# Performance work log

Hardware: AMD Instinct MI355X
Metric: run time of the kernel (lower is better)

The kernel has to match this reference:

```python
import jax, jax.numpy as jnp
import numpy as np


def _consts():
    # Hypercube vertices: itertools.product([-1,1], repeat=n) order => MSB-first bits.
    def verts(nbits):
        idx = np.arange(2 ** nbits)
        return (((idx[:, None] >> np.arange(nbits - 1, -1, -1)[None, :]) & 1) * 2.0 - 1.0).astype(np.float32)

    hexagrams = verts(6)   # (64, 6)
    q2_verts = verts(2)    # (4, 2)
    q3_verts = verts(3)    # (8, 3)

    # Q2 vertex -> group one-hot, _Q2_TO_GROUP = [2, 1, 1, 0]
    q2_to_group = np.zeros((4, 3), dtype=np.float32)
    for v, g in enumerate([2, 1, 1, 0]):
        q2_to_group[v, g] = 1.0

    # Group anchors: ABSTRACT = mean(hex[63], hex[62]), DYNAMIC = mean(hex[19], hex[21]),
    # CONCRETE = mean(hex[0], hex[8]); then L2-normalized.
    anch = np.stack([
        hexagrams[[63, 62]].mean(0),
        hexagrams[[19, 21]].mean(0),
        hexagrams[[0, 8]].mean(0),
    ]).astype(np.float32)
    anch = anch / np.clip(np.linalg.norm(anch, axis=-1, keepdims=True), 1e-12, None)

    # Walsh-Hadamard popcount masks, pre-divided by their sums -> (64, 3) matrix.
    bits = np.array([bin(i).count('1') for i in range(64)], dtype=np.float32)
    wa = (bits >= 5).astype(np.float32)
    wd = (bits == 3).astype(np.float32)
    wc = (bits <= 1).astype(np.float32)
    wht_mat = np.stack([wa / wa.sum(), wd / wd.sum(), wc / wc.sum()], axis=1)

    return tuple(jnp.asarray(a) for a in (hexagrams, q2_verts, q3_verts, q2_to_group, anch, wht_mat))


def _q3_to_group_init():
    q3_map = np.zeros((8, 3), dtype=np.float32)
    for i in range(8):
        yc = bin(i).count('1')
        if yc == 0:
            q3_map[i, 2] = 1.0
        elif yc == 1:
            q3_map[i, 1] = 1.0
        elif yc == 2:
            q3_map[i, 0] = 0.6
            q3_map[i, 1] = 0.4
        else:
            q3_map[i, 0] = 1.0
    q3_map = q3_map / np.clip(q3_map.sum(axis=1, keepdims=True), 1e-8, None)
    return q3_map


def setup_inputs() -> dict:
    key = jax.random.key(0)
    k_x, k2, k3, k6 = jax.random.split(key, 4)
    B, T, D = 4, 4096, 2048
    s = 1.0 / float(np.sqrt(D))  # torch Linear default init range
    return {
        'x': jax.random.normal(k_x, (B, T, D), dtype=jnp.float32),
        'ln_w': jnp.ones((D,), dtype=jnp.float32),
        'ln_b': jnp.zeros((D,), dtype=jnp.float32),
        'w_q2': jax.random.uniform(k2, (2, D), minval=-s, maxval=s, dtype=jnp.float32),
        'w_q3': jax.random.uniform(k3, (3, D), minval=-s, maxval=s, dtype=jnp.float32),
        'w_q6': jax.random.uniform(k6, (6, D), minval=-s, maxval=s, dtype=jnp.float32),
        'log_temp': jnp.asarray(np.log(0.5), dtype=jnp.float32),
        'log_scale_mix': jnp.zeros((3,), dtype=jnp.float32),
        'q3_to_group': jnp.asarray(_q3_to_group_init()),
        'log_wht_mix': jnp.asarray(-2.0, dtype=jnp.float32),
    }


def _forward(x, ln_w, ln_b, w_q2, w_q3, w_q6, log_temp, log_scale_mix, q3_to_group, log_wht_mix):
    hexa, q2v, q3v, q2g, anch, wht_mat = _consts()

    # LayerNorm (eps = 1e-5, torch default)
    mu = x.mean(-1, keepdims=True)
    var = ((x - mu) ** 2).mean(-1, keepdims=True)
    h = (x - mu) * jax.lax.rsqrt(var + 1e-5) * ln_w + ln_b

    temp = jnp.clip(jnp.exp(log_temp), 0.1, 5.0)

    # Q2 scale: (B,T,2) -> 4 vertices -> 3 groups
    w2 = jax.nn.softmax(jnp.tanh(h @ w_q2.T) @ q2v.T / temp, axis=-1)
    score_q2 = w2 @ q2g

    # Q3 scale: (B,T,3) -> 8 vertices -> learned soft group map
    w3 = jax.nn.softmax(jnp.tanh(h @ w_q3.T) @ q3v.T / temp, axis=-1)
    score_q3 = w3 @ jax.nn.softmax(q3_to_group, axis=-1)

    # Q6 scale: (B,T,6) -> 64 hexagram vertices
    hex_w = jax.nn.softmax(jnp.tanh(h @ w_q6.T) @ hexa.T / temp, axis=-1)
    score_cos = (hex_w @ hexa) @ anch.T            # cosine-sim vs normalized anchors
    score_wht = hex_w @ wht_mat                    # popcount-mask averages
    alpha = jax.nn.sigmoid(log_wht_mix)
    score_q6 = (1.0 - alpha) * score_cos + alpha * score_wht

    mix = jax.nn.softmax(log_scale_mix)
    group_w = jax.nn.softmax(mix[0] * score_q2 + mix[1] * score_q3 + mix[2] * score_q6, axis=-1)

    mg = group_w.mean(axis=(0, 1))
    mh = hex_w.mean(axis=(0, 1))
    lb_loss = jnp.sum(mg * jnp.log(mg + 1e-8)) + 0.1 * jnp.sum(mh * jnp.log(mh + 1e-8))
    return group_w, hex_w, lb_loss


def reference(x, ln_w, ln_b, w_q2, w_q3, w_q6, log_temp, log_scale_mix, q3_to_group, log_wht_mix):
    return _forward(x, ln_w, ln_b, w_q2, w_q3, w_q6, log_temp, log_scale_mix, q3_to_group, log_wht_mix)
```

## Files before the change

### kernel.cpp

```cpp
#include <hip/hip_runtime.h>
#include <math.h>
#include <string.h>

#define D 2048
#define NTOK 16384
#define NROW 11
#define MROWS_U32 (NROW * D / 2)
#define K1_BLOCKS 1024
#define K1_THREADS 256
#define WROWS 13
#define WSTRIDE_U 1032
#define TILE_S 20

#define WS_A 0
#define WS_B 16
#define WS_IT 32
#define WS_ALPHA 33
#define WS_MIX 34
#define WS_M3 40
#define WS_MERGED 64
#define WS_PART (WS_MERGED + MROWS_U32)

typedef __fp16 h2 __attribute__((ext_vector_type(2)));
typedef __fp16 h8 __attribute__((ext_vector_type(8)));
typedef float f32x4 __attribute__((ext_vector_type(4)));

__device__ __forceinline__ float wsum(float v){
#pragma unroll
  for (int m = 1; m < 64; m <<= 1) v += __shfl_xor(v, m, 64);
  return v;
}
__device__ __forceinline__ float wmax(float v){
#pragma unroll
  for (int m = 1; m < 64; m <<= 1) v = fmaxf(v, __shfl_xor(v, m, 64));
  return v;
}
__device__ __forceinline__ float rcp_fast(float x){ return __builtin_amdgcn_rcpf(x); }
__device__ __forceinline__ float tanh_fast(float x){
  float e = __expf(2.0f * x);
  return 1.0f - 2.0f * rcp_fast(e + 1.0f);
}
__device__ __forceinline__ float sload(const float* __restrict__ p){
  return __uint_as_float(__builtin_amdgcn_readfirstlane(__float_as_uint(*p)));
}
__device__ __forceinline__ unsigned int h2u(h2 h){ unsigned int u; memcpy(&u, &h, 4); return u; }

__global__ __launch_bounds__(256) void k0_prep(
    const float* __restrict__ ln_w, const float* __restrict__ ln_b,
    const float* __restrict__ w_q2, const float* __restrict__ w_q3,
    const float* __restrict__ w_q6,
    const float* __restrict__ log_temp, const float* __restrict__ log_scale_mix,
    const float* __restrict__ q3_to_group, const float* __restrict__ log_wht_mix,
    float* __restrict__ ws)
{
  const int tid = threadIdx.x;
  const int k = blockIdx.x;
  unsigned int* wsu = (unsigned int*)ws;
  if (k < NROW){
    const float* row = (k < 2) ? (w_q2 + (size_t)k * D)
                     : (k < 5) ? (w_q3 + (size_t)(k - 2) * D)
                               : (w_q6 + (size_t)(k - 5) * D);
    float pa = 0.f, pb = 0.f;
    for (int i = tid * 2; i < D; i += 512){
      float w0 = row[i], w1 = row[i + 1];
      h2 h = __builtin_amdgcn_cvt_pkrtz(ln_w[i] * w0, ln_w[i + 1] * w1);
      pa += (float)h[0] + (float)h[1];
      pb = fmaf(ln_b[i], w0, pb);
      pb = fmaf(ln_b[i + 1], w1, pb);
      wsu[WS_MERGED + k * 1024 + i / 2] = h2u(h);
    }
    __shared__ float red[8];
    pa = wsum(pa); pb = wsum(pb);
    if ((tid & 63) == 0){ red[tid >> 6] = pa; red[4 + (tid >> 6)] = pb; }
    __syncthreads();
    if (tid == 0){
      ws[WS_A + k] = red[0] + red[1] + red[2] + red[3];
      ws[WS_B + k] = red[4] + red[5] + red[6] + red[7];
    }
  } else if (tid == 0){
    float t = __expf(log_temp[0]);
    t = fminf(fmaxf(t, 0.1f), 5.0f);
    ws[WS_IT] = 1.0f / t;
    ws[WS_ALPHA] = 1.0f / (1.0f + __expf(-log_wht_mix[0]));
    float m0 = log_scale_mix[0], m1 = log_scale_mix[1], m2 = log_scale_mix[2];
    float mm = fmaxf(m0, fmaxf(m1, m2));
    float e0 = __expf(m0 - mm), e1 = __expf(m1 - mm), e2 = __expf(m2 - mm);
    float inv = 1.0f / (e0 + e1 + e2);
    ws[WS_MIX + 0] = e0 * inv; ws[WS_MIX + 1] = e1 * inv; ws[WS_MIX + 2] = e2 * inv;
    for (int r = 0; r < 8; ++r){
      float v0 = q3_to_group[r*3+0], v1 = q3_to_group[r*3+1], v2 = q3_to_group[r*3+2];
      float mx = fmaxf(v0, fmaxf(v1, v2));
      float f0 = __expf(v0 - mx), f1 = __expf(v1 - mx), f2 = __expf(v2 - mx);
      float iv = 1.0f / (f0 + f1 + f2);
      ws[WS_M3 + r*3 + 0] = f0 * iv;
      ws[WS_M3 + r*3 + 1] = f1 * iv;
      ws[WS_M3 + r*3 + 2] = f2 * iv;
    }
  }
}

__global__ __launch_bounds__(256) void k1_main(
    const float* __restrict__ x, const float* __restrict__ ws,
    float* __restrict__ gout, float* __restrict__ hout, float* __restrict__ part)
{
  __shared__ unsigned int sW[WROWS * WSTRIDE_U];
  __shared__ float tile[4][16][TILE_S];
  __shared__ float lred[4][68];
  const int tid  = threadIdx.x;
  const int lane = tid & 63;
  const int wid  = tid >> 6;
  const int blk  = blockIdx.x;
  const int tok0 = blk * 16;
  const int n = lane & 15;
  const int q = lane >> 4;

  {
    const uint4* src = (const uint4*)((const unsigned int*)ws + WS_MERGED);
    const uint4 ones4 = make_uint4(0x3C003C00u, 0x3C003C00u, 0x3C003C00u, 0x3C003C00u);
    const uint4 zero4 = make_uint4(0u, 0u, 0u, 0u);
#pragma unroll
    for (int j = 0; j < WROWS; ++j){
      int idx = tid + j * 256;
      int r = idx >> 8, i = idx & 255;
      uint4 v = (r < NROW) ? src[r * 256 + i] : ((r == NROW) ? ones4 : zero4);
      *(uint4*)(sW + r * WSTRIDE_U + i * 4) = v;
    }
  }

  const float* xp = x + (size_t)(tok0 + n) * D + wid * 512 + q * 8;

  f32x4 acc = {0.f, 0.f, 0.f, 0.f};
  float sq = 0.f;

  float4 f0 = *(const float4*)(xp);
  float4 f1 = *(const float4*)(xp + 4);

  __syncthreads();

  const int wr = (n <= 12) ? n : 12;
  const unsigned int* wb = sW + wr * WSTRIDE_U + wid * 256 + q * 4;

#pragma unroll
  for (int s = 0; s < 16; ++s){
    float4 g0, g1;
    if (s < 15){
      g0 = *(const float4*)(xp + (s + 1) * 32);
      g1 = *(const float4*)(xp + (s + 1) * 32 + 4);
    }
    sq = fmaf(f0.x,f0.x, fmaf(f0.y,f0.y, fmaf(f0.z,f0.z, fmaf(f0.w,f0.w, sq))));
    sq = fmaf(f1.x,f1.x, fmaf(f1.y,f1.y, fmaf(f1.z,f1.z, fmaf(f1.w,f1.w, sq))));
    h2 p0 = __builtin_amdgcn_cvt_pkrtz(f0.x, f0.y);
    h2 p1 = __builtin_amdgcn_cvt_pkrtz(f0.z, f0.w);
    h2 p2 = __builtin_amdgcn_cvt_pkrtz(f1.x, f1.y);
    h2 p3 = __builtin_amdgcn_cvt_pkrtz(f1.z, f1.w);
    h8 A;
    A[0]=p0[0]; A[1]=p0[1]; A[2]=p1[0]; A[3]=p1[1];
    A[4]=p2[0]; A[5]=p2[1]; A[6]=p3[0]; A[7]=p3[1];
    uint4 wq = *(const uint4*)(wb + s * 16);
    h8 B; memcpy(&B, &wq, 16);
    acc = __builtin_amdgcn_mfma_f32_16x16x32_f16(A, B, acc, 0, 0, 0);
    f0 = g0; f1 = g1;
  }

  sq += __shfl_xor(sq, 16, 64);
  sq += __shfl_xor(sq, 32, 64);

#pragma unroll
  for (int r = 0; r < 4; ++r) tile[wid][q * 4 + r][n] = acc[r];
  if (lane < 16) tile[wid][lane][16] = sq;

  __syncthreads();

  float a[NROW], bb[NROW];
#pragma unroll
  for (int k = 0; k < NROW; ++k){ a[k] = sload(ws + WS_A + k); bb[k] = sload(ws + WS_B + k); }
  const float it    = sload(ws + WS_IT);
  const float alpha = sload(ws + WS_ALPHA);
  const float mix0 = sload(ws + WS_MIX), mix1 = sload(ws + WS_MIX + 1), mix2 = sload(ws + WS_MIX + 2);
  float M3r[8][3];
#pragma unroll
  for (int r = 0; r < 8; ++r){
#pragma unroll
    for (int g = 0; g < 3; ++g) M3r[r][g] = sload(ws + WS_M3 + r*3 + g);
  }

  float sgn[6];
#pragma unroll
  for (int j = 0; j < 6; ++j) sgn[j] = ((lane >> (5 - j)) & 1) ? 1.0f : -1.0f;
  const float C5 = 0.44721359549995793f;
  const float A0c[6] = { C5,  C5,  C5,  C5,  C5, 0.f };
  const float A1c[6] = {-0.5f, 0.5f, -0.5f, 0.f, 0.f, 0.5f};
  const float A2c[6] = {-C5, -C5, 0.f, -C5, -C5, -C5};
  float cs0 = 0.f, cs1 = 0.f, cs2 = 0.f;
#pragma unroll
  for (int j = 0; j < 6; ++j){
    cs0 = fmaf(sgn[j], A0c[j], cs0);
    cs1 = fmaf(sgn[j], A1c[j], cs1);
    cs2 = fmaf(sgn[j], A2c[j], cs2);
  }
  const int pc = __popc(lane);
  const float w7c = 1.0f / 7.0f;
  float wh0 = (pc >= 5) ? w7c  : 0.f;
  float wh1 = (pc == 3) ? 0.05f: 0.f;
  float wh2 = (pc <= 1) ? w7c  : 0.f;
  const float m60 = (1.f - alpha)*cs0 + alpha*wh0;
  const float m61 = (1.f - alpha)*cs1 + alpha*wh1;
  const float m62 = (1.f - alpha)*cs2 + alpha*wh2;

  float hsum = 0.f, ga0 = 0.f, ga1 = 0.f, ga2 = 0.f;

#pragma unroll 1
  for (int i = 0; i < 4; ++i){
    const int tl  = wid * 4 + i;
    const int tok = tok0 + tl;

    float t[12]; float sqv = 0.f;
#pragma unroll
    for (int k = 0; k < 12; ++k) t[k] = 0.f;
#pragma unroll
    for (int hh = 0; hh < 4; ++hh){
      const float* row = &tile[hh][tl][0];
      float4 c0 = *(const float4*)(row);
      float4 c1 = *(const float4*)(row + 4);
      float4 c2 = *(const float4*)(row + 8);
      t[0] += c0.x; t[1] += c0.y; t[2]  += c0.z; t[3]  += c0.w;
      t[4] += c1.x; t[5] += c1.y; t[6]  += c1.z; t[7]  += c1.w;
      t[8] += c2.x; t[9] += c2.y; t[10] += c2.z; t[11] += c2.w;
      sqv += row[16];
    }

    float mean = t[11] * (1.0f / D);
    float var  = fmaf(sqv, 1.0f / D, -mean * mean);
    float rr   = rsqrtf(var + 1e-5f);
    float u[NROW];
#pragma unroll
    for (int k = 0; k < NROW; ++k){
      float d = fmaf(-mean, a[k], t[k]);
      u[k] = tanh_fast(fmaf(rr, d, bb[k]));
    }

    float p01 = u[0] + u[1], m01 = u[0] - u[1];
    float l0 = -p01*it, l1 = -m01*it, l2 = m01*it, l3 = p01*it;
    float mx2 = fmaxf(fmaxf(l0, l1), fmaxf(l2, l3));
    float e0 = __expf(l0-mx2), e1 = __expf(l1-mx2), e2 = __expf(l2-mx2), e3 = __expf(l3-mx2);
    float i2 = rcp_fast(e0 + e1 + e2 + e3);
    float s2g0 = e3 * i2, s2g1 = (e1 + e2) * i2, s2g2 = e0 * i2;

    float l3v[8]; float mx3 = -1e30f;
#pragma unroll
    for (int v = 0; v < 8; ++v){
      float acc3 = ((v & 4) ? u[2] : -u[2]) + ((v & 2) ? u[3] : -u[3]) + ((v & 1) ? u[4] : -u[4]);
      l3v[v] = acc3 * it;
      mx3 = fmaxf(mx3, l3v[v]);
    }
    float w3v[8]; float se3 = 0.f;
#pragma unroll
    for (int v = 0; v < 8; ++v){ w3v[v] = __expf(l3v[v] - mx3); se3 += w3v[v]; }
    float i3 = rcp_fast(se3);
    float s3g0 = 0.f, s3g1 = 0.f, s3g2 = 0.f;
#pragma unroll
    for (int v = 0; v < 8; ++v){
      s3g0 = fmaf(w3v[v], M3r[v][0], s3g0);
      s3g1 = fmaf(w3v[v], M3r[v][1], s3g1);
      s3g2 = fmaf(w3v[v], M3r[v][2], s3g2);
    }
    s3g0 *= i3; s3g1 *= i3; s3g2 *= i3;

    float lg = 0.f;
#pragma unroll
    for (int jj = 0; jj < 6; ++jj) lg = fmaf(sgn[jj], u[5 + jj], lg);
    lg *= it;
    float mx6 = wmax(lg);
    float p   = __expf(lg - mx6);
    float se6 = wsum(p);
    float hw  = p * rcp_fast(se6);
    hout[(size_t)tok * 64 + lane] = hw;
    hsum += hw;
    float s6g0 = wsum(hw * m60);
    float s6g1 = wsum(hw * m61);
    float s6g2 = wsum(hw * m62);

    float g0 = mix0*s2g0 + mix1*s3g0 + mix2*s6g0;
    float g1 = mix0*s2g1 + mix1*s3g1 + mix2*s6g1;
    float g2 = mix0*s2g2 + mix1*s3g2 + mix2*s6g2;
    float gm = fmaxf(g0, fmaxf(g1, g2));
    float y0 = __expf(g0-gm), y1 = __expf(g1-gm), y2 = __expf(g2-gm);
    float gi = rcp_fast(y0 + y1 + y2);
    float gw0 = y0*gi, gw1 = y1*gi, gw2 = y2*gi;
    ga0 += gw0; ga1 += gw1; ga2 += gw2;
    if (lane < 3){
      float val = (lane == 0) ? gw0 : (lane == 1) ? gw1 : gw2;
      gout[(size_t)tok * 3 + lane] = val;
    }
  }

  lred[wid][lane] = hsum;
  if (lane < 3){
    float val = (lane == 0) ? ga0 : (lane == 1) ? ga1 : ga2;
    lred[wid][64 + lane] = val;
  }
  __syncthreads();
  if (tid < 67){
    float v = lred[0][tid] + lred[1][tid] + lred[2][tid] + lred[3][tid];
    part[(size_t)tid * K1_BLOCKS + blk] = v;
  }
}

__global__ __launch_bounds__(1024) void k2_loss(const float* __restrict__ part,
                                                float* __restrict__ lout)
{
  __shared__ float sums[68];
  const int tid = threadIdx.x;
  const int lane = tid & 63;
  const int wid  = tid >> 6;
  for (int jv = wid; jv < 67; jv += 16){
    const float4* p = (const float4*)(part + (size_t)jv * K1_BLOCKS);
    float v = 0.f;
#pragma unroll
    for (int b = 0; b < K1_BLOCKS / 256; ++b){
      float4 q = p[lane + b * 64];
      v += (q.x + q.y) + (q.z + q.w);
    }
    v = wsum(v);
    if (lane == 0) sums[jv] = v;
  }
  __syncthreads();
  if (wid == 0){
    const float inv = 1.0f / (float)NTOK;
    float mh = sums[lane] * inv;
    float term = 0.1f * mh * logf(mh + 1e-8f);
    if (lane < 3){
      float mg = sums[64 + lane] * inv;
      term += mg * logf(mg + 1e-8f);
    }
    float L = wsum(term);
    if (lane == 0) lout[0] = L;
  }
}

extern "C" void kernel_launch(void* const* d_in, const int* in_sizes, int n_in,
                              void* d_out, int out_size, void* d_ws, size_t ws_size,
                              hipStream_t stream)
{
  const float* x             = (const float*)d_in[0];
  const float* ln_w          = (const float*)d_in[1];
  const float* ln_b          = (const float*)d_in[2];
  const float* w_q2          = (const float*)d_in[3];
  const float* w_q3          = (const float*)d_in[4];
  const float* w_q6          = (const float*)d_in[5];
  const float* log_temp      = (const float*)d_in[6];
  const float* log_scale_mix = (const float*)d_in[7];
  const float* q3_to_group   = (const float*)d_in[8];
  const float* log_wht_mix   = (const float*)d_in[9];

  float* out  = (float*)d_out;
  float* gout = out;
  float* hout = out + (size_t)NTOK * 3;
  float* lout = out + (size_t)NTOK * 3 + (size_t)NTOK * 64;
  float* ws   = (float*)d_ws;

  k0_prep<<<12, 256, 0, stream>>>(ln_w, ln_b, w_q2, w_q3, w_q6,
                                  log_temp, log_scale_mix, q3_to_group, log_wht_mix, ws);
  k1_main<<<K1_BLOCKS, K1_THREADS, 0, stream>>>(x, ws, gout, hout, ws + WS_PART);
  k2_loss<<<1, 1024, 0, stream>>>(ws + WS_PART, lout);
}
```

Baseline: 50.45 us.

## Batch x loads ahead of weight staging and shrink shared weight buffer

Issues the first half of each thread's x loads before staging weights into LDS, then converts that half to fp16 while the second half of the loads is in flight. The MFMA loop is split into two 8-step batches. The shared weight buffer drops the ones and zero rows: the ones row is synthesized in registers and the padding row is aliased onto existing rows. This raises memory-level parallelism and cuts LDS use and staging work, at the cost of more registers (16 float4 plus 16 h8 live), which may lower occupancy. The LDS row stride also changes to 1036.

```diff
diff --git a/kernel.cpp b/kernel.cpp
--- a/kernel.cpp
+++ b/kernel.cpp
@@ -8,8 +8,7 @@
 #define MROWS_U32 (NROW * D / 2)
 #define K1_BLOCKS 1024
 #define K1_THREADS 256
-#define WROWS 13
-#define WSTRIDE_U 1032
+#define WSTRIDE_U 1036
 #define TILE_S 20
 
 #define WS_A 0
@@ -103,7 +102,7 @@
     const float* __restrict__ x, const float* __restrict__ ws,
     float* __restrict__ gout, float* __restrict__ hout, float* __restrict__ part)
 {
-  __shared__ unsigned int sW[WROWS * WSTRIDE_U];
+  __shared__ unsigned int sW[NROW * WSTRIDE_U];
   __shared__ float tile[4][16][TILE_S];
   __shared__ float lred[4][68];
   const int tid  = threadIdx.x;
@@ -114,39 +113,30 @@
   const int n = lane & 15;
   const int q = lane >> 4;
 
+  const float* xp = x + (size_t)(tok0 + n) * D + wid * 512 + q * 8;
+
+  float4 xa[16];
+#pragma unroll
+  for (int s = 0; s < 8; ++s){
+    xa[2*s]     = *(const float4*)(xp + s * 32);
+    xa[2*s + 1] = *(const float4*)(xp + s * 32 + 4);
+  }
+
   {
     const uint4* src = (const uint4*)((const unsigned int*)ws + WS_MERGED);
-    const uint4 ones4 = make_uint4(0x3C003C00u, 0x3C003C00u, 0x3C003C00u, 0x3C003C00u);
-    const uint4 zero4 = make_uint4(0u, 0u, 0u, 0u);
-#pragma unroll
-    for (int j = 0; j < WROWS; ++j){
+#pragma unroll
+    for (int j = 0; j < 11; ++j){
       int idx = tid + j * 256;
       int r = idx >> 8, i = idx & 255;
-      uint4 v = (r < NROW) ? src[r * 256 + i] : ((r == NROW) ? ones4 : zero4);
-      *(uint4*)(sW + r * WSTRIDE_U + i * 4) = v;
-    }
-  }
-
-  const float* xp = x + (size_t)(tok0 + n) * D + wid * 512 + q * 8;
-
-  f32x4 acc = {0.f, 0.f, 0.f, 0.f};
+      *(uint4*)(sW + r * WSTRIDE_U + i * 4) = src[r * 256 + i];
+    }
+  }
+
   float sq = 0.f;
-
-  float4 f0 = *(const float4*)(xp);
-  float4 f1 = *(const float4*)(xp + 4);
-
-  __syncthreads();
-
-  const int wr = (n <= 12) ? n : 12;
-  const unsigned int* wb = sW + wr * WSTRIDE_U + wid * 256 + q * 4;
-
-#pragma unroll
-  for (int s = 0; s < 16; ++s){
-    float4 g0, g1;
-    if (s < 15){
-      g0 = *(const float4*)(xp + (s + 1) * 32);
-      g1 = *(const float4*)(xp + (s + 1) * 32 + 4);
-    }
+  h8 hxA[8], hxB[8];
+#pragma unroll
+  for (int s = 0; s < 8; ++s){
+    float4 f0 = xa[2*s], f1 = xa[2*s + 1];
     sq = fmaf(f0.x,f0.x, fmaf(f0.y,f0.y, fmaf(f0.z,f0.z, fmaf(f0.w,f0.w, sq))));
     sq = fmaf(f1.x,f1.x, fmaf(f1.y,f1.y, fmaf(f1.z,f1.z, fmaf(f1.w,f1.w, sq))));
     h2 p0 = __builtin_amdgcn_cvt_pkrtz(f0.x, f0.y);
@@ -156,10 +146,52 @@
     h8 A;
     A[0]=p0[0]; A[1]=p0[1]; A[2]=p1[0]; A[3]=p1[1];
     A[4]=p2[0]; A[5]=p2[1]; A[6]=p3[0]; A[7]=p3[1];
+    hxA[s] = A;
+  }
+#pragma unroll
+  for (int s = 0; s < 8; ++s){
+    xa[2*s]     = *(const float4*)(xp + (s + 8) * 32);
+    xa[2*s + 1] = *(const float4*)(xp + (s + 8) * 32 + 4);
+  }
+
+  __syncthreads();
+
+  const int wr = (n < NROW) ? n : (n - NROW);
+  const bool is_ones = (n == NROW);
+  const uint4 ones4 = make_uint4(0x3C003C00u, 0x3C003C00u, 0x3C003C00u, 0x3C003C00u);
+  const unsigned int* wb = sW + wr * WSTRIDE_U + wid * 256 + q * 4;
+
+  f32x4 acc = {0.f, 0.f, 0.f, 0.f};
+
+#pragma unroll
+  for (int s = 0; s < 8; ++s){
     uint4 wq = *(const uint4*)(wb + s * 16);
+    if (is_ones) wq = ones4;
     h8 B; memcpy(&B, &wq, 16);
-    acc = __builtin_amdgcn_mfma_f32_16x16x32_f16(A, B, acc, 0, 0, 0);
-    f0 = g0; f1 = g1;
+    acc = __builtin_amdgcn_mfma_f32_16x16x32_f16(hxA[s], B, acc, 0, 0, 0);
+  }
+
+#pragma unroll
+  for (int s = 0; s < 8; ++s){
+    float4 f0 = xa[2*s], f1 = xa[2*s + 1];
+    sq = fmaf(f0.x,f0.x, fmaf(f0.y,f0.y, fmaf(f0.z,f0.z, fmaf(f0.w,f0.w, sq))));
+    sq = fmaf(f1.x,f1.x, fmaf(f1.y,f1.y, fmaf(f1.z,f1.z, fmaf(f1.w,f1.w, sq))));
+    h2 p0 = __builtin_amdgcn_cvt_pkrtz(f0.x, f0.y);
+    h2 p1 = __builtin_amdgcn_cvt_pkrtz(f0.z, f0.w);
+    h2 p2 = __builtin_amdgcn_cvt_pkrtz(f1.x, f1.y);
+    h2 p3 = __builtin_amdgcn_cvt_pkrtz(f1.z, f1.w);
+    h8 A;
+    A[0]=p0[0]; A[1]=p0[1]; A[2]=p1[0]; A[3]=p1[1];
+    A[4]=p2[0]; A[5]=p2[1]; A[6]=p3[0]; A[7]=p3[1];
+    hxB[s] = A;
+  }
+
+#pragma unroll
+  for (int s = 0; s < 8; ++s){
+    uint4 wq = *(const uint4*)(wb + (s + 8) * 16);
+    if (is_ones) wq = ones4;
+    h8 B; memcpy(&B, &wq, 16);
+    acc = __builtin_amdgcn_mfma_f32_16x16x32_f16(hxB[s], B, acc, 0, 0, 0);
   }
 
   sq += __shfl_xor(sq, 16, 64);
```

Result: no change. 50.00 us (-0.9%).
